# Optimization experiments

Hardware: AMD Instinct MI355X
Metric: run time of the kernel (lower is better)

Reference implementation:

```python
import jax, jax.numpy as jnp
import numpy as np

N_HEAD = 16
NEG_BIG = 1e10  # matches the module's -10000000000.0 masking constant


def setup_inputs() -> dict:
    key = jax.random.key(0)
    k1, k2, k3 = jax.random.split(key, 3)
    B, S, D = 2, 2048, 1024
    std = 0.02
    return {
        "x": jax.random.normal(k1, (B, S, D), dtype=jnp.float32),
        "c_attn_w": jax.random.normal(k2, (D, 3 * D), dtype=jnp.float32) * std,
        "c_attn_b": jnp.zeros((3 * D,), dtype=jnp.float32),
        "c_proj_w": jax.random.normal(k3, (D, D), dtype=jnp.float32) * std,
        "c_proj_b": jnp.zeros((D,), dtype=jnp.float32),
    }


def reference(x, c_attn_w, c_attn_b, c_proj_w, c_proj_b):
    B, S, D = x.shape
    H = N_HEAD
    Dh = D // H

    # c_attn: fused QKV projection (Conv1D == linear)
    qkv = jnp.einsum("bsd,df->bsf", x, c_attn_w) + c_attn_b  # [B,S,3D]
    q, k, v = jnp.split(qkv, 3, axis=-1)

    def split_heads(t):  # [B,S,D] -> [B,H,S,Dh]
        return t.reshape(B, S, H, Dh).transpose(0, 2, 1, 3)

    q, k, v = split_heads(q), split_heads(k), split_heads(v)
    present = jnp.stack([k, v], axis=1)  # [B,2,H,S,Dh]

    # scores: explicit O(S^2) matrix, scaled by sqrt(head_dim)
    w = jnp.einsum("bhqd,bhkd->bhqk", q, k) / jnp.sqrt(
        jnp.asarray(Dh, dtype=q.dtype)
    )  # [B,H,S,S]

    # causal mask, applied exactly as in the source: w*mask - 1e10*(1-mask)
    mask = jnp.tril(jnp.ones((S, S), dtype=w.dtype))[None, None]  # [1,1,S,S]
    w = w * mask - NEG_BIG * (1.0 - mask)

    w = jax.nn.softmax(w, axis=-1)
    a = jnp.einsum("bhqk,bhkd->bhqd", w, v)  # [B,H,S,Dh]

    # merge heads: [B,H,S,Dh] -> [B,S,D]
    a = a.transpose(0, 2, 1, 3).reshape(B, S, D)

    # output projection
    a = jnp.einsum("bsd,df->bsf", a, c_proj_w) + c_proj_b
    return (a, present)
```

## Files before the change

kernel.cpp:

```cpp
#include <hip/hip_runtime.h>
#include <hip/hip_bf16.h>
#include <stdint.h>

typedef __bf16 bf16_t;
typedef __bf16 bf16x8 __attribute__((ext_vector_type(8)));
typedef __bf16 bf16x4v __attribute__((ext_vector_type(4)));
typedef float f32x4 __attribute__((ext_vector_type(4)));

#define MFMA16(A, B, C) __builtin_amdgcn_mfma_f32_16x16x32_bf16((A), (B), (C), 0, 0, 0)

#define BB 2
#define SS 2048
#define DD 1024
#define HH 16
#define DH 64
#define MM (BB * SS)

__device__ __forceinline__ void load_lds16(const void* g, void* l) {
  __builtin_amdgcn_global_load_lds(
      (const __attribute__((address_space(1))) void*)g,
      (__attribute__((address_space(3))) void*)l, 16, 0, 0);
}


__global__ __launch_bounds__(256) void cvt_f32_to_bf16(const float* __restrict__ in,
                                                       bf16_t* __restrict__ out, int n4) {
  int i = blockIdx.x * blockDim.x + threadIdx.x;
  if (i >= n4) return;
  float4 v = reinterpret_cast<const float4*>(in)[i];
  bf16x4v o;
  o[0] = (bf16_t)v.x; o[1] = (bf16_t)v.y; o[2] = (bf16_t)v.z; o[3] = (bf16_t)v.w;
  reinterpret_cast<bf16x4v*>(out)[i] = o;
}

__global__ void transpose_f32_to_bf16(const float* __restrict__ W, bf16_t* __restrict__ WT,
                                      int K, int N) {
  __shared__ float tile[32][33];
  int n0 = blockIdx.x * 32, k0 = blockIdx.y * 32;
  int tx = threadIdx.x, ty = threadIdx.y;
  #pragma unroll
  for (int i = ty; i < 32; i += 8) tile[i][tx] = W[(size_t)(k0 + i) * N + n0 + tx];
  __syncthreads();
  #pragma unroll
  for (int i = ty; i < 32; i += 8) WT[(size_t)(n0 + i) * K + k0 + tx] = (bf16_t)tile[tx][i];
}

template <int EPI>
__global__ __launch_bounds__(256) void gemm_bf16(
    const bf16_t* __restrict__ A, const bf16_t* __restrict__ BT,
    const float* __restrict__ bias, float* __restrict__ outf,
    bf16_t* __restrict__ q_b, bf16_t* __restrict__ k_b, bf16_t* __restrict__ vt_b,
    int M, int N, int K) {
  __shared__ __align__(16) bf16_t At[2][128 * 32];
  __shared__ __align__(16) bf16_t Bt[2][128 * 32];

  const int tid = threadIdx.x;
  const int l = tid & 63, w = tid >> 6;
  const int lr = l & 15, lg = l >> 4;
  const int wr = w >> 1, wc = w & 1;
  const int row0 = blockIdx.y * 128, col0 = blockIdx.x * 128;

  auto stage = [&](int buf, int k0) {
    #pragma unroll
    for (int i = 0; i < 2; ++i) {
      int e = (tid + i * 256) * 8;
      int r = e >> 5, c = e & 31;
      int base = (w * 64 + i * 256) * 8;
      load_lds16(&A[(size_t)(row0 + r) * K + k0 + c], &At[buf][base]);
      load_lds16(&BT[(size_t)(col0 + r) * K + k0 + c], &Bt[buf][base]);
    }
  };

  f32x4 vz = {0.f, 0.f, 0.f, 0.f};
  f32x4 acc[4][4];
  #pragma unroll
  for (int m = 0; m < 4; ++m)
    #pragma unroll
    for (int n = 0; n < 4; ++n) acc[m][n] = vz;

  stage(0, 0);
  __syncthreads();
  int cur = 0;
  for (int k0 = 0; k0 < K; k0 += 32) {
    if (k0 + 32 < K) stage(cur ^ 1, k0 + 32);
    bf16x8 af[4], bfr[4];
    #pragma unroll
    for (int m = 0; m < 4; ++m)
      af[m] = *(const bf16x8*)&At[cur][(wr * 64 + m * 16 + lr) * 32 + lg * 8];
    #pragma unroll
    for (int n = 0; n < 4; ++n)
      bfr[n] = *(const bf16x8*)&Bt[cur][(wc * 64 + n * 16 + lr) * 32 + lg * 8];
    #pragma unroll
    for (int m = 0; m < 4; ++m)
      #pragma unroll
      for (int n = 0; n < 4; ++n) acc[m][n] = MFMA16(af[m], bfr[n], acc[m][n]);
    __syncthreads();
    cur ^= 1;
  }

  #pragma unroll
  for (int m = 0; m < 4; ++m) {
    int rl = wr * 64 + m * 16 + lg * 4;
    #pragma unroll
    for (int n = 0; n < 4; ++n) {
      int col = col0 + wc * 64 + n * 16 + lr;
      float bz = bias[col];
      #pragma unroll
      for (int r = 0; r < 4; ++r) {
        int row = row0 + rl + r;
        float v = acc[m][n][r] + bz;
        if (EPI == 1) {
          outf[(size_t)row * N + col] = v;
        } else {
          int b = row >> 11, s = row & 2047;
          int part = col >> 10, d = col & 1023;
          int h = d >> 6, dh = d & 63;
          size_t idx = ((size_t)(b * HH + h) * SS + s) * DH + dh;
          if (part == 0) {
            q_b[idx] = (bf16_t)v;
          } else if (part == 1) {
            k_b[idx] = (bf16_t)v;
            outf[(((size_t)(b * 2 + 0) * HH + h) * SS + s) * DH + dh] = v;
          } else {
            vt_b[((size_t)(b * HH + h) * DH + dh) * SS + s] = (bf16_t)v;
            outf[(((size_t)(b * 2 + 1) * HH + h) * SS + s) * DH + dh] = v;
          }
        }
      }
    }
  }
}

__global__ __launch_bounds__(256) void attn_fwd(
    const bf16_t* __restrict__ q_b, const bf16_t* __restrict__ k_b,
    const bf16_t* __restrict__ vt_b, bf16_t* __restrict__ attn_out) {
  __shared__ __align__(16) bf16_t Kt[2][64 * 64];
  __shared__ __align__(16) bf16_t Vt[2][64 * 64];
  __shared__ __align__(16) bf16_t P_lds[4][32][72];

  const int bh = blockIdx.y;
  const int q0b = (gridDim.x - 1 - blockIdx.x) * 128;
  const int tid = threadIdx.x;
  const int w = tid >> 6, l = tid & 63;
  const int lr = l & 15, lg = l >> 4;

  const bf16_t* qb = q_b + (size_t)bh * SS * DH;
  const bf16_t* kb = k_b + (size_t)bh * SS * DH;
  const bf16_t* vt = vt_b + (size_t)bh * DH * SS;

  auto stageKV = [&](int buf, int kv0) {
    #pragma unroll
    for (int i = 0; i < 2; ++i) {
      int e = (tid + i * 256) * 8;
      int r = e >> 6;
      int cs = (((e & 63) * 2) ^ ((r & 7) << 4)) >> 1;
      int base = (w * 64 + i * 256) * 8;
      load_lds16(&kb[(size_t)(kv0 + r) * DH + cs], &Kt[buf][base]);
      load_lds16(&vt[(size_t)r * SS + kv0 + cs], &Vt[buf][base]);
    }
  };

  const int qrow0 = q0b + w * 32 + lr;
  const int qrow1 = qrow0 + 16;
  bf16x8 qf[2][2];
  qf[0][0] = *(const bf16x8*)&qb[(size_t)qrow0 * DH + lg * 8];
  qf[0][1] = *(const bf16x8*)&qb[(size_t)qrow0 * DH + 32 + lg * 8];
  qf[1][0] = *(const bf16x8*)&qb[(size_t)qrow1 * DH + lg * 8];
  qf[1][1] = *(const bf16x8*)&qb[(size_t)qrow1 * DH + 32 + lg * 8];

  f32x4 vzero = {0.f, 0.f, 0.f, 0.f};
  f32x4 oacc[2][4];
  #pragma unroll
  for (int q = 0; q < 2; ++q)
    #pragma unroll
    for (int d = 0; d < 4; ++d) oacc[q][d] = vzero;
  float m_run[2] = {-1e30f, -1e30f}, l_run[2] = {0.f, 0.f};

  const float SCL = 0.125f * 1.4426950408889634f;

  const int nkv = q0b / 64 + 2;
  stageKV(0, 0);
  __syncthreads();
  int cur = 0;
  for (int t = 0; t < nkv; ++t) {
    const int kv0 = t * 64;
    if (t + 1 < nkv) stageKV(cur ^ 1, (t + 1) * 64);

    float sc[2][4][4];
    #pragma unroll
    for (int kvf = 0; kvf < 4; ++kvf) {
      int rr = kvf * 16 + lr;
      int sw = (rr & 7) << 4;
      const char* kbase = (const char*)&Kt[cur][0] + rr * 128;
      bf16x8 kf0 = *(const bf16x8*)(kbase + ((lg * 16) ^ sw));
      bf16x8 kf1 = *(const bf16x8*)(kbase + ((64 + lg * 16) ^ sw));
      #pragma unroll
      for (int q = 0; q < 2; ++q) {
        f32x4 a = vzero;
        a = MFMA16(kf0, qf[q][0], a);
        a = MFMA16(kf1, qf[q][1], a);
        #pragma unroll
        for (int r = 0; r < 4; ++r) sc[q][kvf][r] = a[r] * SCL;
      }
    }
    if (kv0 + 63 > q0b + w * 32) {
      #pragma unroll
      for (int q = 0; q < 2; ++q) {
        int qrow = q ? qrow1 : qrow0;
        #pragma unroll
        for (int kvf = 0; kvf < 4; ++kvf)
          #pragma unroll
          for (int r = 0; r < 4; ++r) {
            int kv = kv0 + kvf * 16 + lg * 4 + r;
            if (kv > qrow) sc[q][kvf][r] = -3.0e9f;
          }
      }
    }

    #pragma unroll
    for (int q = 0; q < 2; ++q) {
      float tmax = -1e30f;
      #pragma unroll
      for (int kvf = 0; kvf < 4; ++kvf)
        #pragma unroll
        for (int r = 0; r < 4; ++r) tmax = fmaxf(tmax, sc[q][kvf][r]);
      tmax = fmaxf(tmax, __shfl_xor(tmax, 16));
      tmax = fmaxf(tmax, __shfl_xor(tmax, 32));
      if (!__all(tmax <= m_run[q] + 8.0f)) {
        float mnew = fmaxf(m_run[q], tmax);
        float alpha = exp2f(m_run[q] - mnew);
        l_run[q] *= alpha;
        #pragma unroll
        for (int d = 0; d < 4; ++d) oacc[q][d] *= alpha;
        m_run[q] = mnew;
      }
      float mq = m_run[q];
      float psum = 0.f;
      #pragma unroll
      for (int kvf = 0; kvf < 4; ++kvf)
        #pragma unroll
        for (int r = 0; r < 4; ++r) {
          float p = exp2f(sc[q][kvf][r] - mq);
          sc[q][kvf][r] = p;
          psum += p;
        }
      psum += __shfl_xor(psum, 16);
      psum += __shfl_xor(psum, 32);
      l_run[q] += psum;
      #pragma unroll
      for (int kvf = 0; kvf < 4; ++kvf) {
        bf16x4v pk;
        #pragma unroll
        for (int r = 0; r < 4; ++r) pk[r] = (bf16_t)sc[q][kvf][r];
        *(bf16x4v*)&P_lds[w][q * 16 + lr][kvf * 16 + lg * 4] = pk;
      }
    }

    bf16x8 pf[2][2];
    #pragma unroll
    for (int q = 0; q < 2; ++q) {
      pf[q][0] = *(const bf16x8*)&P_lds[w][q * 16 + lr][lg * 8];
      pf[q][1] = *(const bf16x8*)&P_lds[w][q * 16 + lr][32 + lg * 8];
    }
    #pragma unroll
    for (int d = 0; d < 4; ++d) {
      int dl = d * 16 + lr;
      int sw = (dl & 7) << 4;
      const char* vbase = (const char*)&Vt[cur][0] + dl * 128;
      bf16x8 vf0 = *(const bf16x8*)(vbase + ((lg * 16) ^ sw));
      bf16x8 vf1 = *(const bf16x8*)(vbase + ((64 + lg * 16) ^ sw));
      #pragma unroll
      for (int q = 0; q < 2; ++q) {
        oacc[q][d] = MFMA16(vf0, pf[q][0], oacc[q][d]);
        oacc[q][d] = MFMA16(vf1, pf[q][1], oacc[q][d]);
      }
    }
    __syncthreads();
    cur ^= 1;
  }

  const int b = bh >> 4, h = bh & 15;
  #pragma unroll
  for (int q = 0; q < 2; ++q) {
    float inv_l = 1.f / l_run[q];
    int qrow = q ? qrow1 : qrow0;
    #pragma unroll
    for (int d = 0; d < 4; ++d)
      #pragma unroll
      for (int r = 0; r < 4; ++r) {
        int dd = d * 16 + lg * 4 + r;
        attn_out[((size_t)(b * SS + qrow)) * DD + h * DH + dd] =
            (bf16_t)(oacc[q][d][r] * inv_l);
      }
  }
}

extern "C" void kernel_launch(void* const* d_in, const int* in_sizes, int n_in,
                              void* d_out, int out_size, void* d_ws, size_t ws_size,
                              hipStream_t stream) {
  const float* x = (const float*)d_in[0];
  const float* c_attn_w = (const float*)d_in[1];
  const float* c_attn_b = (const float*)d_in[2];
  const float* c_proj_w = (const float*)d_in[3];
  const float* c_proj_b = (const float*)d_in[4];

  float* out = (float*)d_out;
  float* present = out + (size_t)BB * SS * DD;

  char* ws = (char*)d_ws;
  bf16_t* xb     = (bf16_t*)(ws + 0);
  bf16_t* wqkvT  = (bf16_t*)(ws + 8388608);
  bf16_t* wprojT = (bf16_t*)(ws + 14680064);
  bf16_t* q_b    = (bf16_t*)(ws + 16777216);
  bf16_t* k_b    = (bf16_t*)(ws + 25165824);
  bf16_t* vt_b   = (bf16_t*)(ws + 33554432);
  bf16_t* attn_o = (bf16_t*)(ws + 41943040);

  cvt_f32_to_bf16<<<(MM * DD / 4 + 255) / 256, 256, 0, stream>>>(x, xb, MM * DD / 4);
  transpose_f32_to_bf16<<<dim3(3 * DD / 32, DD / 32), dim3(32, 8), 0, stream>>>(
      c_attn_w, wqkvT, DD, 3 * DD);
  transpose_f32_to_bf16<<<dim3(DD / 32, DD / 32), dim3(32, 8), 0, stream>>>(
      c_proj_w, wprojT, DD, DD);
  gemm_bf16<0><<<dim3(3 * DD / 128, MM / 128), 256, 0, stream>>>(
      xb, wqkvT, c_attn_b, present, q_b, k_b, vt_b, MM, 3 * DD, DD);
  attn_fwd<<<dim3(SS / 128, BB * HH), 256, 0, stream>>>(q_b, k_b, vt_b, attn_o);
  gemm_bf16<1><<<dim3(DD / 128, MM / 128), 256, 0, stream>>>(
      attn_o, wprojT, c_proj_b, out, nullptr, nullptr, nullptr, MM, DD, DD);
}
```

Before: 245.4 us.

## Triple-buffer LDS staging with partial vmcnt waits in GEMM and attention

Both the GEMM and the attention kernel move from double to triple LDS buffering and prefetch two stages ahead. The full __syncthreads is replaced by an explicit s_waitcnt vmcnt(4) plus barrier, so the most recent stage's async global-to-LDS loads can stay in flight while the oldest stage is consumed. This should hide more global memory latency. The cost is 50% more LDS per block, which can lower occupancy, and correctness now depends on the hand-coded vmcnt count matching the four loads issued per stage.

```diff
diff --git a/kernel.cpp b/kernel.cpp
--- a/kernel.cpp
+++ b/kernel.cpp
@@ -21,6 +21,19 @@
       (const __attribute__((address_space(1))) void*)g,
       (__attribute__((address_space(3))) void*)l, 16, 0, 0);
 }
+
+#define PIPE_BARRIER_KEEP4()                                            \
+  do {                                                                  \
+    asm volatile("s_waitcnt vmcnt(4) lgkmcnt(0)" ::: "memory");         \
+    __builtin_amdgcn_sched_barrier(0);                                  \
+    __builtin_amdgcn_s_barrier();                                       \
+  } while (0)
+#define PIPE_BARRIER_DRAIN()                                            \
+  do {                                                                  \
+    asm volatile("s_waitcnt vmcnt(0) lgkmcnt(0)" ::: "memory");         \
+    __builtin_amdgcn_sched_barrier(0);                                  \
+    __builtin_amdgcn_s_barrier();                                       \
+  } while (0)
 
 
 __global__ __launch_bounds__(256) void cvt_f32_to_bf16(const float* __restrict__ in,
@@ -51,8 +64,8 @@
     const float* __restrict__ bias, float* __restrict__ outf,
     bf16_t* __restrict__ q_b, bf16_t* __restrict__ k_b, bf16_t* __restrict__ vt_b,
     int M, int N, int K) {
-  __shared__ __align__(16) bf16_t At[2][128 * 32];
-  __shared__ __align__(16) bf16_t Bt[2][128 * 32];
+  __shared__ __align__(16) bf16_t At[3][128 * 32];
+  __shared__ __align__(16) bf16_t Bt[3][128 * 32];
 
   const int tid = threadIdx.x;
   const int l = tid & 63, w = tid >> 6;
@@ -78,24 +91,29 @@
     #pragma unroll
     for (int n = 0; n < 4; ++n) acc[m][n] = vz;
 
+  const int nk = K / 32;
   stage(0, 0);
-  __syncthreads();
-  int cur = 0;
-  for (int k0 = 0; k0 < K; k0 += 32) {
-    if (k0 + 32 < K) stage(cur ^ 1, k0 + 32);
+  stage(1, 32);
+  PIPE_BARRIER_KEEP4();
+  int b0 = 0, b1 = 1, b2 = 2;
+  for (int k = 0; k < nk; ++k) {
+    if (k + 2 < nk) stage(b2, (k + 2) * 32);
     bf16x8 af[4], bfr[4];
     #pragma unroll
     for (int m = 0; m < 4; ++m)
-      af[m] = *(const bf16x8*)&At[cur][(wr * 64 + m * 16 + lr) * 32 + lg * 8];
+      af[m] = *(const bf16x8*)&At[b0][(wr * 64 + m * 16 + lr) * 32 + lg * 8];
     #pragma unroll
     for (int n = 0; n < 4; ++n)
-      bfr[n] = *(const bf16x8*)&Bt[cur][(wc * 64 + n * 16 + lr) * 32 + lg * 8];
+      bfr[n] = *(const bf16x8*)&Bt[b0][(wc * 64 + n * 16 + lr) * 32 + lg * 8];
     #pragma unroll
     for (int m = 0; m < 4; ++m)
       #pragma unroll
       for (int n = 0; n < 4; ++n) acc[m][n] = MFMA16(af[m], bfr[n], acc[m][n]);
-    __syncthreads();
-    cur ^= 1;
+    if (k + 1 < nk) {
+      if (k + 2 < nk) PIPE_BARRIER_KEEP4();
+      else            PIPE_BARRIER_DRAIN();
+    }
+    int t = b0; b0 = b1; b1 = b2; b2 = t;
   }
 
   #pragma unroll
@@ -134,8 +152,8 @@
 __global__ __launch_bounds__(256) void attn_fwd(
     const bf16_t* __restrict__ q_b, const bf16_t* __restrict__ k_b,
     const bf16_t* __restrict__ vt_b, bf16_t* __restrict__ attn_out) {
-  __shared__ __align__(16) bf16_t Kt[2][64 * 64];
-  __shared__ __align__(16) bf16_t Vt[2][64 * 64];
+  __shared__ __align__(16) bf16_t Kt[3][64 * 64];
+  __shared__ __align__(16) bf16_t Vt[3][64 * 64];
   __shared__ __align__(16) bf16_t P_lds[4][32][72];
 
   const int bh = blockIdx.y;
@@ -180,18 +198,19 @@
 
   const int nkv = q0b / 64 + 2;
   stageKV(0, 0);
-  __syncthreads();
-  int cur = 0;
+  stageKV(1, 64);
+  PIPE_BARRIER_KEEP4();
+  int b0 = 0, b1 = 1, b2 = 2;
   for (int t = 0; t < nkv; ++t) {
     const int kv0 = t * 64;
-    if (t + 1 < nkv) stageKV(cur ^ 1, (t + 1) * 64);
+    if (t + 2 < nkv) stageKV(b2, (t + 2) * 64);
 
     float sc[2][4][4];
     #pragma unroll
     for (int kvf = 0; kvf < 4; ++kvf) {
       int rr = kvf * 16 + lr;
       int sw = (rr & 7) << 4;
-      const char* kbase = (const char*)&Kt[cur][0] + rr * 128;
+      const char* kbase = (const char*)&Kt[b0][0] + rr * 128;
       bf16x8 kf0 = *(const bf16x8*)(kbase + ((lg * 16) ^ sw));
       bf16x8 kf1 = *(const bf16x8*)(kbase + ((64 + lg * 16) ^ sw));
       #pragma unroll
@@ -266,7 +285,7 @@
     for (int d = 0; d < 4; ++d) {
       int dl = d * 16 + lr;
       int sw = (dl & 7) << 4;
-      const char* vbase = (const char*)&Vt[cur][0] + dl * 128;
+      const char* vbase = (const char*)&Vt[b0][0] + dl * 128;
       bf16x8 vf0 = *(const bf16x8*)(vbase + ((lg * 16) ^ sw));
       bf16x8 vf1 = *(const bf16x8*)(vbase + ((64 + lg * 16) ^ sw));
       #pragma unroll
@@ -275,8 +294,11 @@
         oacc[q][d] = MFMA16(vf1, pf[q][1], oacc[q][d]);
       }
     }
-    __syncthreads();
-    cur ^= 1;
+    if (t + 1 < nkv) {
+      if (t + 2 < nkv) PIPE_BARRIER_KEEP4();
+      else             PIPE_BARRIER_DRAIN();
+    }
+    int tmp = b0; b0 = b1; b1 = b2; b2 = tmp;
   }
 
   const int b = bh >> 4, h = bh & 15;
```

Measured after the change: 248.0 us. Within noise of the previous version (+1.0%).

## Streamline attention softmax: raw exp, packed bf16 convert, MFMA row sums, fold scaling

Applied to the files above, without the earlier changes.

Reworks the attention inner loop in several ways. Score scaling is folded into an FMA inside the exponent, and the exponent uses raw v_exp_f32. P is packed to bf16 with v_cvt_pk_bf16_f32, and the row-sum shuffle reduction is replaced by an MFMA against a ones vector on the bf16 P values. It also precomputes the LDS swizzle offsets and global staging pointers, and relaxes the lazy-rescale threshold to 44 in unscaled units. This trims VALU and shuffle work in the softmax, at the cost of extra MFMAs and a row sum taken from bf16-rounded probabilities, which may slightly change accuracy.

```diff
diff --git a/kernel.cpp b/kernel.cpp
--- a/kernel.cpp
+++ b/kernel.cpp
@@ -20,6 +20,17 @@
   __builtin_amdgcn_global_load_lds(
       (const __attribute__((address_space(1))) void*)g,
       (__attribute__((address_space(3))) void*)l, 16, 0, 0);
+}
+
+__device__ __forceinline__ float fast_exp2(float x) {
+  float r;
+  asm("v_exp_f32 %0, %1" : "=v"(r) : "v"(x));
+  return r;
+}
+__device__ __forceinline__ uint32_t cvt_pk_bf16(float lo, float hi) {
+  uint32_t u;
+  asm("v_cvt_pk_bf16_f32 %0, %1, %2" : "=v"(u) : "v"(lo), "v"(hi));
+  return u;
 }
 
 
@@ -148,16 +159,20 @@
   const bf16_t* kb = k_b + (size_t)bh * SS * DH;
   const bf16_t* vt = vt_b + (size_t)bh * DH * SS;
 
-  auto stageKV = [&](int buf, int kv0) {
-    #pragma unroll
-    for (int i = 0; i < 2; ++i) {
-      int e = (tid + i * 256) * 8;
-      int r = e >> 6;
-      int cs = (((e & 63) * 2) ^ ((r & 7) << 4)) >> 1;
-      int base = (w * 64 + i * 256) * 8;
-      load_lds16(&kb[(size_t)(kv0 + r) * DH + cs], &Kt[buf][base]);
-      load_lds16(&vt[(size_t)r * SS + kv0 + cs], &Vt[buf][base]);
-    }
+  const int r0 = tid >> 3;
+  const int cs = (((tid & 7) * 16) ^ ((r0 & 7) << 4)) >> 1;
+  const bf16_t* gk0 = kb + r0 * DH + cs;
+  const bf16_t* gk1 = gk0 + 32 * DH;
+  const bf16_t* gv0 = vt + (size_t)r0 * SS + cs;
+  const bf16_t* gv1 = gv0 + 32 * SS;
+  auto stageKV = [&](int buf) {
+    bf16_t* lk = &Kt[buf][w * 512];
+    load_lds16(gk0, lk);
+    load_lds16(gk1, lk + 2048);
+    bf16_t* lv = &Vt[buf][w * 512];
+    load_lds16(gv0, lv);
+    load_lds16(gv1, lv + 2048);
+    gk0 += 64 * DH; gk1 += 64 * DH; gv0 += 64; gv1 += 64;
   };
 
   const int qrow0 = q0b + w * 32 + lr;
@@ -168,6 +183,10 @@
   qf[1][0] = *(const bf16x8*)&qb[(size_t)qrow1 * DH + lg * 8];
   qf[1][1] = *(const bf16x8*)&qb[(size_t)qrow1 * DH + 32 + lg * 8];
 
+  bf16x8 ones;
+  #pragma unroll
+  for (int j = 0; j < 8; ++j) ones[j] = (bf16_t)1.0f;
+
   f32x4 vzero = {0.f, 0.f, 0.f, 0.f};
   f32x4 oacc[2][4];
   #pragma unroll
@@ -177,82 +196,78 @@
   float m_run[2] = {-1e30f, -1e30f}, l_run[2] = {0.f, 0.f};
 
   const float SCL = 0.125f * 1.4426950408889634f;
+  const int sw = (lr & 7) << 4;
+  const int rd0 = (lg * 16) ^ sw;
+  const int rd1 = (64 + lg * 16) ^ sw;
 
   const int nkv = q0b / 64 + 2;
-  stageKV(0, 0);
+  stageKV(0);
   __syncthreads();
   int cur = 0;
   for (int t = 0; t < nkv; ++t) {
     const int kv0 = t * 64;
-    if (t + 1 < nkv) stageKV(cur ^ 1, (t + 1) * 64);
+    if (t + 1 < nkv) stageKV(cur ^ 1);
 
     float sc[2][4][4];
     #pragma unroll
     for (int kvf = 0; kvf < 4; ++kvf) {
-      int rr = kvf * 16 + lr;
-      int sw = (rr & 7) << 4;
-      const char* kbase = (const char*)&Kt[cur][0] + rr * 128;
-      bf16x8 kf0 = *(const bf16x8*)(kbase + ((lg * 16) ^ sw));
-      bf16x8 kf1 = *(const bf16x8*)(kbase + ((64 + lg * 16) ^ sw));
+      const char* kbase = (const char*)&Kt[cur][0] + (kvf * 16 + lr) * 128;
+      bf16x8 kf0 = *(const bf16x8*)(kbase + rd0);
+      bf16x8 kf1 = *(const bf16x8*)(kbase + rd1);
       #pragma unroll
       for (int q = 0; q < 2; ++q) {
         f32x4 a = vzero;
         a = MFMA16(kf0, qf[q][0], a);
         a = MFMA16(kf1, qf[q][1], a);
         #pragma unroll
-        for (int r = 0; r < 4; ++r) sc[q][kvf][r] = a[r] * SCL;
+        for (int r = 0; r < 4; ++r) sc[q][kvf][r] = a[r];
       }
     }
     if (kv0 + 63 > q0b + w * 32) {
       #pragma unroll
       for (int q = 0; q < 2; ++q) {
-        int qrow = q ? qrow1 : qrow0;
+        int dthr = (q ? qrow1 : qrow0) - kv0;
         #pragma unroll
         for (int kvf = 0; kvf < 4; ++kvf)
           #pragma unroll
           for (int r = 0; r < 4; ++r) {
-            int kv = kv0 + kvf * 16 + lg * 4 + r;
-            if (kv > qrow) sc[q][kvf][r] = -3.0e9f;
+            int kvl = kvf * 16 + lg * 4 + r;
+            if (kvl > dthr) sc[q][kvf][r] = -1e30f;
           }
       }
     }
 
     #pragma unroll
     for (int q = 0; q < 2; ++q) {
-      float tmax = -1e30f;
-      #pragma unroll
-      for (int kvf = 0; kvf < 4; ++kvf)
-        #pragma unroll
-        for (int r = 0; r < 4; ++r) tmax = fmaxf(tmax, sc[q][kvf][r]);
-      tmax = fmaxf(tmax, __shfl_xor(tmax, 16));
-      tmax = fmaxf(tmax, __shfl_xor(tmax, 32));
-      if (!__all(tmax <= m_run[q] + 8.0f)) {
-        float mnew = fmaxf(m_run[q], tmax);
-        float alpha = exp2f(m_run[q] - mnew);
+      float tm = fmaxf(fmaxf(sc[q][0][0], sc[q][0][1]), sc[q][0][2]);
+      tm = fmaxf(fmaxf(tm, sc[q][0][3]), sc[q][1][0]);
+      tm = fmaxf(fmaxf(tm, sc[q][1][1]), sc[q][1][2]);
+      tm = fmaxf(fmaxf(tm, sc[q][1][3]), sc[q][2][0]);
+      tm = fmaxf(fmaxf(tm, sc[q][2][1]), sc[q][2][2]);
+      tm = fmaxf(fmaxf(tm, sc[q][2][3]), sc[q][3][0]);
+      tm = fmaxf(fmaxf(tm, sc[q][3][1]), sc[q][3][2]);
+      tm = fmaxf(tm, sc[q][3][3]);
+      tm = fmaxf(tm, __shfl_xor(tm, 16));
+      tm = fmaxf(tm, __shfl_xor(tm, 32));
+      if (!__all(tm <= m_run[q] + 44.0f)) {
+        float mnew = fmaxf(m_run[q], tm);
+        float alpha = fast_exp2((m_run[q] - mnew) * SCL);
         l_run[q] *= alpha;
         #pragma unroll
         for (int d = 0; d < 4; ++d) oacc[q][d] *= alpha;
         m_run[q] = mnew;
       }
-      float mq = m_run[q];
-      float psum = 0.f;
-      #pragma unroll
-      for (int kvf = 0; kvf < 4; ++kvf)
-        #pragma unroll
-        for (int r = 0; r < 4; ++r) {
-          float p = exp2f(sc[q][kvf][r] - mq);
-          sc[q][kvf][r] = p;
-          psum += p;
-        }
-      psum += __shfl_xor(psum, 16);
-      psum += __shfl_xor(psum, 32);
-      l_run[q] += psum;
+      float mneg = m_run[q] * (-SCL);
       #pragma unroll
       for (int kvf = 0; kvf < 4; ++kvf) {
-        bf16x4v pk;
-        #pragma unroll
-        for (int r = 0; r < 4; ++r) pk[r] = (bf16_t)sc[q][kvf][r];
-        *(bf16x4v*)&P_lds[w][q * 16 + lr][kvf * 16 + lg * 4] = pk;
+        float p0 = fast_exp2(__builtin_fmaf(sc[q][kvf][0], SCL, mneg));
+        float p1 = fast_exp2(__builtin_fmaf(sc[q][kvf][1], SCL, mneg));
+        float p2 = fast_exp2(__builtin_fmaf(sc[q][kvf][2], SCL, mneg));
+        float p3 = fast_exp2(__builtin_fmaf(sc[q][kvf][3], SCL, mneg));
+        uint2 pk;
+        pk.x = cvt_pk_bf16(p0, p1);
+        pk.y = cvt_pk_bf16(p2, p3);
+        *(uint2*)&P_lds[w][q * 16 + lr][kvf * 16 + lg * 4] = pk;
       }
     }
 
@@ -261,14 +276,16 @@
     for (int q = 0; q < 2; ++q) {
       pf[q][0] = *(const bf16x8*)&P_lds[w][q * 16 + lr][lg * 8];
       pf[q][1] = *(const bf16x8*)&P_lds[w][q * 16 + lr][32 + lg * 8];
+      f32x4 ls = vzero;
+      ls = MFMA16(ones, pf[q][0], ls);
+      ls = MFMA16(ones, pf[q][1], ls);
+      l_run[q] += ls[0];
     }
     #pragma unroll
     for (int d = 0; d < 4; ++d) {
-      int dl = d * 16 + lr;
-      int sw = (dl & 7) << 4;
-      const char* vbase = (const char*)&Vt[cur][0] + dl * 128;
-      bf16x8 vf0 = *(const bf16x8*)(vbase + ((lg * 16) ^ sw));
-      bf16x8 vf1 = *(const bf16x8*)(vbase + ((64 + lg * 16) ^ sw));
+      const char* vbase = (const char*)&Vt[cur][0] + (d * 16 + lr) * 128;
+      bf16x8 vf0 = *(const bf16x8*)(vbase + rd0);
+      bf16x8 vf1 = *(const bf16x8*)(vbase + rd1);
       #pragma unroll
       for (int q = 0; q < 2; ++q) {
         oacc[q][d] = MFMA16(vf0, pf[q][0], oacc[q][d]);
```

After: 228.2 us. 1.08x faster.
